# Optimization experiments

Measured on AMD Instinct MI355X. Metric: run time of the kernel, lower is better.

Reference implementation:

```python
import jax, jax.numpy as jnp
import numpy as np

MAX_DISP = 48
PATCH = 3
OFFSET = 0
PAD = PATCH // 2
EPS = 1e-3


def _unfold(x, P, pad):
    # x: [B,C,H,W] -> [B,C,K2,H,W], K2 enumerated row-major over the PxP window
    B, C, H, W = x.shape
    xp = jnp.pad(x, ((0, 0), (0, 0), (pad, pad), (pad, pad)))
    return jnp.stack([xp[:, :, i:i + H, j:j + W]
                      for i in range(P) for j in range(P)], axis=2)


def _normalize(x, axes):
    # torch F.normalize: x / clamp(||x||_2, min=eps)
    n = jnp.sqrt(jnp.sum(x * x, axis=axes, keepdims=True))
    return x / jnp.maximum(n, EPS)


def setup_inputs() -> dict:
    key = jax.random.key(0)
    k1, k2, k3 = jax.random.split(key, 3)
    shp = (2, 32, 128, 416)
    return {
        "xl": jax.random.normal(k1, shp, dtype=jnp.float32),
        "xm": jax.random.normal(k2, shp, dtype=jnp.float32),
        "xr": jax.random.normal(k3, shp, dtype=jnp.float32),
    }


def reference(xl, xm, xr):
    B, C, H, W = xl.shape
    K2 = PATCH * PATCH
    scale = (C * K2) ** 0.5

    pl = _normalize(_unfold(xl, PATCH, PAD), (1, 2))  # [B,C,K2,H,W]
    pr = _normalize(_unfold(xr, PATCH, PAD), (1, 2))
    fl = _normalize(xm, (1,))                          # [B,C,H,W]

    # fl is constant over the K2 axis, so sum patches over K2 once for sim_L/sim_R
    Sl = pl.sum(axis=2)  # [B,C,H,W]
    Sr = pr.sum(axis=2)

    cL, cR, cLR = [], [], []
    for d in range(OFFSET, OFFSET + MAX_DISP):
        if d > 0:
            # shifted_l[w] = patches_l[w+d] (zero right pad); shifted_r[w] = patches_r[w-d]
            sL = jnp.einsum('bchw,bchw->bhw', fl[..., :W - d], Sl[..., d:])
            sL = jnp.pad(sL, ((0, 0), (0, 0), (0, d)))
            sR = jnp.einsum('bchw,bchw->bhw', fl[..., d:], Sr[..., :W - d])
            sR = jnp.pad(sR, ((0, 0), (0, 0), (d, 0)))
            wlr = W - 2 * d  # overlap region of the two opposite shifts
            if wlr > 0:
                sLR = jnp.einsum('bckhw,bckhw->bhw', pl[..., 2 * d:], pr[..., :wlr])
                sLR = jnp.pad(sLR, ((0, 0), (0, 0), (d, d)))
            else:
                sLR = jnp.zeros((B, H, W), xl.dtype)
        else:
            sL = jnp.einsum('bchw,bchw->bhw', fl, Sl)
            sR = jnp.einsum('bchw,bchw->bhw', fl, Sr)
            sLR = jnp.einsum('bckhw,bckhw->bhw', pl, pr)
        cL.append(sL / scale)
        cR.append(sR / scale)
        cLR.append(sLR / scale)

    cost = jnp.stack([jnp.stack(cL, 1), jnp.stack(cR, 1), jnp.stack(cLR, 1)], axis=1)
    return jnp.clip(cost, -10.0, 10.0).astype(jnp.float16)  # [B,3,D,H,W]
```

## Files before the change

### kernel.cpp

```cpp
#include <hip/hip_runtime.h>
#include <math.h>

#define B 2
#define C 32
#define H 128
#define W 416
#define D 48
#define HW (H*W)
#define CHW (C*HW)
#define EPSN 1e-3f
#define ISCALE 0.05892556509887896f
#define ESTR 36
#define DSPL (D / 2)

typedef _Float16 h16;
typedef _Float16 __attribute__((ext_vector_type(2))) h16x2;

__device__ __forceinline__ float clip10(float x) {
    return fminf(fmaxf(x, -10.0f), 10.0f);
}

__device__ __forceinline__ float fdot2(h16x2 a, h16x2 bb, float c) {
    return __builtin_amdgcn_fdot2(a, bb, c, false);
}
__device__ __forceinline__ h16x2 u2h(unsigned int u) {
    union { unsigned int u; h16x2 h; } cv; cv.u = u; return cv.h;
}
__device__ __forceinline__ unsigned int pkh(float a, float bb) {
    union { h16x2 h; unsigned int u; } cv;
    cv.h = h16x2{(h16)a, (h16)bb}; return cv.u;
}

#define FMA4(acc, f, k, u) acc += f[4*(k)+0]*(u).x + f[4*(k)+1]*(u).y \
                               + f[4*(k)+2]*(u).z + f[4*(k)+3]*(u).w;

#define CLW(v) ((v) < 0 ? 0 : ((v) > (W - 1) ? (W - 1) : (v)))

__global__ __launch_bounds__(256) void k_norm(const float* __restrict__ sql,
                                              const float* __restrict__ sqr,
                                              float* __restrict__ inl,
                                              float* __restrict__ inr) {
    int idx = blockIdx.x * 256 + threadIdx.x;
    if (idx >= B * HW) return;
    int b = idx / HW, hw = idx - b * HW;
    int h = hw / W, w = hw - h * W;
    float sl = 0.f, sr = 0.f;
#pragma unroll
    for (int di = -1; di <= 1; ++di) {
        int hh = h + di;
        if (hh < 0 || hh >= H) continue;
#pragma unroll
        for (int dj = -1; dj <= 1; ++dj) {
            int ww = w + dj;
            if (ww < 0 || ww >= W) continue;
            int p = b * HW + hh * W + ww;
            sl += sql[p];
            sr += sqr[p];
        }
    }
    inl[idx] = 1.0f / fmaxf(sqrtf(sl), EPSN);
    inr[idx] = 1.0f / fmaxf(sqrtf(sr), EPSN);
}

__device__ __forceinline__ void stage_row_v2(const float* __restrict__ gsrc,
                                             float* __restrict__ lds,
                                             int tid, int nthreads) {
    for (int t = tid; t < (W / 4) * C; t += nthreads) {
        int rw = t & 7;
        int cl = (t >> 3) & 7;
        int g  = t >> 6;
        int wg = g % 13;
        int ch = g / 13;
        int c  = ch * 8 + cl;
        int w4 = (wg * 8 + rw) * 4;
        float4 v = *(const float4*)(gsrc + (size_t)c * HW + w4);
        lds[(w4 + 0) * ESTR + c] = v.x;
        lds[(w4 + 1) * ESTR + c] = v.y;
        lds[(w4 + 2) * ESTR + c] = v.z;
        lds[(w4 + 3) * ESTR + c] = v.w;
    }
}

__device__ __forceinline__ void stage_row3_h(const float* __restrict__ gsrc,
                                             unsigned int* __restrict__ lds,
                                             int h, int tid, int nthreads) {
    for (int t = tid; t < (W / 4) * (C / 2); t += nthreads) {
        int p = t & 15;
        int u = t >> 4;
        int v0 = 4 * u;
        const float* pa = gsrc + (size_t)(2 * p) * HW + v0;
        const float* pb = pa + HW;
        float4 va = *(const float4*)pa;
        float4 vb = *(const float4*)pb;
        if (h > 0) {
            float4 xa = *(const float4*)(pa - W);
            float4 xb = *(const float4*)(pb - W);
            va.x += xa.x; va.y += xa.y; va.z += xa.z; va.w += xa.w;
            vb.x += xb.x; vb.y += xb.y; vb.z += xb.z; vb.w += xb.w;
        }
        if (h < H - 1) {
            float4 xa = *(const float4*)(pa + W);
            float4 xb = *(const float4*)(pb + W);
            va.x += xa.x; va.y += xa.y; va.z += xa.z; va.w += xa.w;
            vb.x += xb.x; vb.y += xb.y; vb.z += xb.z; vb.w += xb.w;
        }
        int q = p >> 2, lo = p & 3;
        unsigned int pk0 = pkh(va.x, vb.x);
        unsigned int pk1 = pkh(va.y, vb.y);
        unsigned int pk2 = pkh(va.z, vb.z);
        unsigned int pk3 = pkh(va.w, vb.w);
#define PUTH(vv, val) { int _v = (vv); \
    lds[16 * (_v ^ ((_v >> 1) & 1)) \
        + 4 * (q ^ ((((_v) >> 1) ^ ((_v) >> 2)) & 3)) + lo] = (val); }
        PUTH(v0 + 0, pk0)
        PUTH(v0 + 1, pk1)
        PUTH(v0 + 2, pk2)
        PUTH(v0 + 3, pk3)
#undef PUTH
    }
}

__device__ __forceinline__ float dot32e(const float* __restrict__ x,
                                        const float* __restrict__ col) {
    const float4* c4 = (const float4*)col;
    float4 u0 = c4[0], u1 = c4[1], u2 = c4[2], u3 = c4[3];
    float4 u4 = c4[4], u5 = c4[5], u6 = c4[6], u7 = c4[7];
    float a = 0.f, bb = 0.f;
    FMA4(a, x, 0, u0) FMA4(a, x, 1, u1) FMA4(a, x, 2, u2) FMA4(a, x, 3, u3)
    FMA4(bb, x, 4, u4) FMA4(bb, x, 5, u5) FMA4(bb, x, 6, u6) FMA4(bb, x, 7, u7)
    return a + bb;
}

__global__ __launch_bounds__(256) void k_lr(const float* __restrict__ xm,
                                            const float* __restrict__ xl,
                                            const float* __restrict__ xr,
                                            const float* __restrict__ inl,
                                            const float* __restrict__ inr,
                                            float* __restrict__ out) {
    __shared__ unsigned int sBu[W * 16];
    __shared__ float sIn[W];
    int tid = threadIdx.x;
    int h = blockIdx.x;
    int b = blockIdx.y;
    int d0 = blockIdx.z * DSPL;
    bool act = tid < (W / 2);
    int w = 2 * tid;
    int bhw = b * HW + h * W;
    const float* pm = xm + (size_t)b * CHW + h * W;

    h16x2 f0h[16], f1h[16];
    if (act) {
        float t0[C], t1[C];
        float am0 = 0.f, am1 = 0.f;
#pragma unroll
        for (int c = 0; c < C; ++c) {
            float2 mv = *(const float2*)(pm + (size_t)c * HW + w);
            t0[c] = mv.x; t1[c] = mv.y;
            am0 += mv.x * mv.x; am1 += mv.y * mv.y;
        }
        float im0 = 1.0f / fmaxf(sqrtf(am0), EPSN);
        float im1 = 1.0f / fmaxf(sqrtf(am1), EPSN);
#pragma unroll
        for (int j = 0; j < 16; ++j) {
            f0h[j] = h16x2{(h16)(t0[2 * j] * im0), (h16)(t0[2 * j + 1] * im0)};
            f1h[j] = h16x2{(h16)(t1[2 * j] * im1), (h16)(t1[2 * j + 1] * im1)};
        }
    } else {
#pragma unroll
        for (int j = 0; j < 16; ++j) { f0h[j] = h16x2{(h16)0.f, (h16)0.f};
                                       f1h[j] = h16x2{(h16)0.f, (h16)0.f}; }
    }

    uint4 RA0, RA1, RA2, RA3;
    uint4 RB0, RB1, RB2, RB3;

#define LOADH(P, vv) { int _v = CLW(vv); \
    const uint4* _c4 = (const uint4*)(sBu + 16 * (_v ^ ((_v >> 1) & 1))); \
    int _ky = ((_v >> 1) ^ (_v >> 2)) & 3; \
    P##0 = _c4[_ky]; P##1 = _c4[1 ^ _ky]; P##2 = _c4[2 ^ _ky]; P##3 = _c4[3 ^ _ky]; }

#define DOTH(P, c0, c1) { \
    float _a0 = 0.f, _a1 = 0.f, _b0 = 0.f, _b1 = 0.f; \
    _a0 = fdot2(f0h[0],  u2h((P##0).x), _a0); _a0 = fdot2(f0h[1],  u2h((P##0).y), _a0); \
    _a0 = fdot2(f0h[2],  u2h((P##0).z), _a0); _a0 = fdot2(f0h[3],  u2h((P##0).w), _a0); \
    _a0 = fdot2(f0h[4],  u2h((P##1).x), _a0); _a0 = fdot2(f0h[5],  u2h((P##1).y), _a0); \
    _a0 = fdot2(f0h[6],  u2h((P##1).z), _a0); _a0 = fdot2(f0h[7],  u2h((P##1).w), _a0); \
    _a1 = fdot2(f0h[8],  u2h((P##2).x), _a1); _a1 = fdot2(f0h[9],  u2h((P##2).y), _a1); \
    _a1 = fdot2(f0h[10], u2h((P##2).z), _a1); _a1 = fdot2(f0h[11], u2h((P##2).w), _a1); \
    _a1 = fdot2(f0h[12], u2h((P##3).x), _a1); _a1 = fdot2(f0h[13], u2h((P##3).y), _a1); \
    _a1 = fdot2(f0h[14], u2h((P##3).z), _a1); _a1 = fdot2(f0h[15], u2h((P##3).w), _a1); \
    _b0 = fdot2(f1h[0],  u2h((P##0).x), _b0); _b0 = fdot2(f1h[1],  u2h((P##0).y), _b0); \
    _b0 = fdot2(f1h[2],  u2h((P##0).z), _b0); _b0 = fdot2(f1h[3],  u2h((P##0).w), _b0); \
    _b0 = fdot2(f1h[4],  u2h((P##1).x), _b0); _b0 = fdot2(f1h[5],  u2h((P##1).y), _b0); \
    _b0 = fdot2(f1h[6],  u2h((P##1).z), _b0); _b0 = fdot2(f1h[7],  u2h((P##1).w), _b0); \
    _b1 = fdot2(f1h[8],  u2h((P##2).x), _b1); _b1 = fdot2(f1h[9],  u2h((P##2).y), _b1); \
    _b1 = fdot2(f1h[10], u2h((P##2).z), _b1); _b1 = fdot2(f1h[11], u2h((P##2).w), _b1); \
    _b1 = fdot2(f1h[12], u2h((P##3).x), _b1); _b1 = fdot2(f1h[13], u2h((P##3).y), _b1); \
    _b1 = fdot2(f1h[14], u2h((P##3).z), _b1); _b1 = fdot2(f1h[15], u2h((P##3).w), _b1); \
    c0 = _a0 + _a1; c1 = _b0 + _b1; }

    stage_row3_h(xl + (size_t)b * CHW + h * W, sBu, h, tid, 256);
    for (int j = tid; j < W; j += 256) sIn[j] = inl[bhw + j];
    __syncthreads();
    if (act) {
        float* oL = out + ((size_t)b * 3 + 0) * D * HW + h * W;
        const int vb = w + d0 - 1;
        float g0a = 0.f, g0b = 0.f, g1a = 0.f, g1b = 0.f, s0p = 0.f;
#define STEPL(P, jj) { int v = vb + (jj); bool ok = (v >= 0) && (v < W); \
    float c0, c1; DOTH(P, c0, c1); c0 = ok ? c0 : 0.f; c1 = ok ? c1 : 0.f; \
    float s0 = 0.f, s1 = 0.f; \
    if ((jj) >= 2) { int m = v - 1; \
        if (m < W) { float sc = sIn[m] * ISCALE; \
            s0 = clip10((g0a + g0b + c0) * sc); s1 = clip10((g1a + g1b + c1) * sc); } \
        if ((jj) >= 3) { int d = d0 + (jj) - 3; \
            *(float2*)(oL + (size_t)d * HW + w) = make_float2(s0p, s1); } } \
    s0p = s0; g0a = g0b; g0b = c0; g1a = g1b; g1b = c1; }
        LOADH(RA, vb);
#pragma unroll 2
        for (int j = 0; j < DSPL + 2; j += 2) {
            LOADH(RB, vb + j + 1);
            STEPL(RA, j);
            LOADH(RA, vb + j + 2);
            STEPL(RB, j + 1);
        }
        STEPL(RA, DSPL + 2);
#undef STEPL
    }
    __syncthreads();

    stage_row3_h(xr + (size_t)b * CHW + h * W, sBu, h, tid, 256);
    for (int j = tid; j < W; j += 256) sIn[j] = inr[bhw + j];
    __syncthreads();
    if (act) {
        float* oR = out + ((size_t)b * 3 + 1) * D * HW + h * W;
        const int vb = w - d0 - DSPL;
        float g0a = 0.f, g0b = 0.f, g1a = 0.f, g1b = 0.f, s0p = 0.f;
#define STEPR(P, jj) { int v = vb + (jj); bool ok = (v >= 0) && (v < W); \
    float c0, c1; DOTH(P, c0, c1); c0 = ok ? c0 : 0.f; c1 = ok ? c1 : 0.f; \
    float s0 = 0.f, s1 = 0.f; \
    if ((jj) >= 2) { int m = v - 1; \
        if (m >= 0) { float sc = sIn[m] * ISCALE; \
            s0 = clip10((g0a + g0b + c0) * sc); s1 = clip10((g1a + g1b + c1) * sc); } \
        if ((jj) >= 3) { int d = d0 + DSPL + 2 - (jj); \
            *(float2*)(oR + (size_t)d * HW + w) = make_float2(s0p, s1); } } \
    s0p = s0; g0a = g0b; g0b = c0; g1a = g1b; g1b = c1; }
        LOADH(RA, vb);
#pragma unroll 2
        for (int j = 0; j < DSPL + 2; j += 2) {
            LOADH(RB, vb + j + 1);
            STEPR(RA, j);
            LOADH(RA, vb + j + 2);
            STEPR(RB, j + 1);
        }
        STEPR(RA, DSPL + 2);
#undef STEPR
    }
#undef LOADH
#undef DOTH
}

__global__ __launch_bounds__(448, 4) void k_e(const float* __restrict__ xl,
                                              const float* __restrict__ xr,
                                              _Float16* __restrict__ EH,
                                              float* __restrict__ sql,
                                              float* __restrict__ sqr) {
    __shared__ float sXL[W * ESTR];
    int tid = threadIdx.x;
    int h = blockIdx.x;
    int b = blockIdx.y;
    int d0 = blockIdx.z * DSPL;
    int lane = tid & 63;
    int wv = tid >> 6;
    int v = wv * 62 + lane - 1;
    bool vin = (v >= 0) && (v < W);
    const float* br = xr + (size_t)b * CHW + h * W;

    float xrv[C];
#pragma unroll
    for (int c = 0; c < C; ++c) xrv[c] = vin ? br[c * HW + v] : 0.0f;

    stage_row_v2(xl + (size_t)b * CHW + h * W, sXL, tid, 448);
    __syncthreads();

    bool wr = (lane >= 1) && (lane <= 62) && (v < W);

    if (blockIdx.z == 0) {
        float sr_ = 0.f, sl_ = 0.f;
#pragma unroll
        for (int c = 0; c < C; ++c) sr_ += xrv[c] * xrv[c];
        if (vin) {
            const float4* c4 = (const float4*)(sXL + v * ESTR);
#pragma unroll
            for (int q = 0; q < 8; ++q) {
                float4 x = c4[q];
                sl_ += x.x * x.x + x.y * x.y + x.z * x.z + x.w * x.w;
            }
        }
        if (wr) {
            sqr[b * HW + h * W + v] = sr_;
            sql[b * HW + h * W + v] = sl_;
        }
    }

    _Float16* pe = EH + (((size_t)b * D) * H + h) * W + v;

    float4 RA0, RA1, RA2, RA3, RA4, RA5, RA6, RA7;
    float4 RB0, RB1, RB2, RB3, RB4, RB5, RB6, RB7;

#define LOADE(P, col) { int _vq = CLW(col); \
    const float4* _c4 = (const float4*)(sXL + (size_t)_vq * ESTR); \
    P##0 = _c4[0]; P##1 = _c4[1]; P##2 = _c4[2]; P##3 = _c4[3]; \
    P##4 = _c4[4]; P##5 = _c4[5]; P##6 = _c4[6]; P##7 = _c4[7]; }
#define STEPE(P, dd) { float _a = 0.f, _b = 0.f; \
    FMA4(_a, xrv, 0, P##0) FMA4(_a, xrv, 1, P##1) FMA4(_a, xrv, 2, P##2) FMA4(_a, xrv, 3, P##3) \
    FMA4(_b, xrv, 4, P##4) FMA4(_b, xrv, 5, P##5) FMA4(_b, xrv, 6, P##6) FMA4(_b, xrv, 7, P##7) \
    float e = (vin && (v + 2 * (dd)) < W) ? (_a + _b) : 0.f; \
    float em = __shfl_up(e, 1); \
    float ep = __shfl_down(e, 1); \
    float eh = em + e + ep; \
    if (wr) pe[(size_t)(dd) * HW] = (_Float16)eh; }

    LOADE(RA, v + 2 * d0);
#pragma unroll 2
    for (int d = d0; d < d0 + DSPL; d += 2) {
        LOADE(RB, v + 2 * d + 2);
        STEPE(RA, d);
        LOADE(RA, v + 2 * d + 4);
        STEPE(RB, d + 1);
    }
#undef LOADE
#undef STEPE
}

#define DCH 12
__global__ __launch_bounds__(448) void k_lr2(const _Float16* __restrict__ EH,
                                             const float* __restrict__ inl,
                                             const float* __restrict__ inr,
                                             float* __restrict__ out) {
    int w = threadIdx.x;
    int dc = blockIdx.x;
    int h = blockIdx.y;
    int b = blockIdx.z;
    if (w >= W) return;
    int bhw = b * HW + h * W;
    bool hm = (h > 0), hp = (h < H - 1);

    float* o = out + ((size_t)b * 3 + 2) * D * HW + h * W + w;
#pragma unroll
    for (int i = 0; i < DCH; ++i) {
        int d = dc * DCH + i;
        float r = 0.0f;
        if (w >= d && w + d < W) {
            int vc = w - d;
            const _Float16* base = EH + ((size_t)b * D + d) * HW + vc;
            float e = (float)base[h * W];
            if (hm) e += (float)base[(h - 1) * W];
            if (hp) e += (float)base[(h + 1) * W];
            float nl = inl[bhw + w + d];
            float nr = inr[bhw + vc];
            r = clip10(e * nl * nr * ISCALE);
        }
        o[(size_t)d * HW] = r;
    }
}

extern "C" void kernel_launch(void* const* d_in, const int* in_sizes, int n_in,
                              void* d_out, int out_size, void* d_ws, size_t ws_size,
                              hipStream_t stream) {
    const float* xl = (const float*)d_in[0];
    const float* xm = (const float*)d_in[1];
    const float* xr = (const float*)d_in[2];
    float* out = (float*)d_out;

    float* ws = (float*)d_ws;
    float* inl = ws;
    float* inr = inl + B * HW;
    float* sql = inr + B * HW;
    float* sqr = sql + B * HW;
    _Float16* EH = (_Float16*)(sqr + B * HW);

    k_e<<<dim3(H, B, 2), dim3(448), 0, stream>>>(xl, xr, EH, sql, sqr);
    k_norm<<<dim3((B * HW + 255) / 256), dim3(256), 0, stream>>>(sql, sqr, inl, inr);
    k_lr<<<dim3(H, B, 2), dim3(256), 0, stream>>>(xm, xl, xr, inl, inr, out);
    k_lr2<<<dim3(4, H, B), dim3(448), 0, stream>>>(EH, inl, inr, out);
}
```

Baseline: 164.3 us.

## Split k_lr into two 256-thread groups computing left and right costs concurrently

k_lr now launches 512 threads per block. It stages both the left and right row patches and their inverse norms into separate shared buffers behind a single barrier. Thread group 0 computes the left-shift cost and group 1 the right-shift cost in parallel, where before they ran one after the other with a restage in between. This removes two barriers and the serial second pass, but doubles shared memory per block, makes each thread recompute the xm normalization, and may lower occupancy through register pressure at launch bounds 512.

```diff
diff --git a/kernel.cpp b/kernel.cpp
--- a/kernel.cpp
+++ b/kernel.cpp
@@ -131,20 +131,24 @@
     return a + bb;
 }
 
-__global__ __launch_bounds__(256) void k_lr(const float* __restrict__ xm,
+__global__ __launch_bounds__(512) void k_lr(const float* __restrict__ xm,
                                             const float* __restrict__ xl,
                                             const float* __restrict__ xr,
                                             const float* __restrict__ inl,
                                             const float* __restrict__ inr,
                                             float* __restrict__ out) {
-    __shared__ unsigned int sBu[W * 16];
-    __shared__ float sIn[W];
+    __shared__ unsigned int sBuL[W * 16];
+    __shared__ unsigned int sBuR[W * 16];
+    __shared__ float sInL[W];
+    __shared__ float sInR[W];
     int tid = threadIdx.x;
+    int grp = tid >> 8;
+    int t8 = tid & 255;
     int h = blockIdx.x;
     int b = blockIdx.y;
     int d0 = blockIdx.z * DSPL;
-    bool act = tid < (W / 2);
-    int w = 2 * tid;
+    bool act = t8 < (W / 2);
+    int w = 2 * t8;
     int bhw = b * HW + h * W;
     const float* pm = xm + (size_t)b * CHW + h * W;
 
@@ -171,11 +175,19 @@
                                        f1h[j] = h16x2{(h16)0.f, (h16)0.f}; }
     }
 
+    stage_row3_h(xl + (size_t)b * CHW + h * W, sBuL, h, tid, 512);
+    stage_row3_h(xr + (size_t)b * CHW + h * W, sBuR, h, tid, 512);
+    for (int j = tid; j < W; j += 512) {
+        sInL[j] = inl[bhw + j];
+        sInR[j] = inr[bhw + j];
+    }
+    __syncthreads();
+
     uint4 RA0, RA1, RA2, RA3;
     uint4 RB0, RB1, RB2, RB3;
 
-#define LOADH(P, vv) { int _v = CLW(vv); \
-    const uint4* _c4 = (const uint4*)(sBu + 16 * (_v ^ ((_v >> 1) & 1))); \
+#define LOADH(P, buf, vv) { int _v = CLW(vv); \
+    const uint4* _c4 = (const uint4*)((buf) + 16 * (_v ^ ((_v >> 1) & 1))); \
     int _ky = ((_v >> 1) ^ (_v >> 2)) & 3; \
     P##0 = _c4[_ky]; P##1 = _c4[1 ^ _ky]; P##2 = _c4[2 ^ _ky]; P##3 = _c4[3 ^ _ky]; }
 
@@ -199,10 +211,7 @@
     _b1 = fdot2(f1h[14], u2h((P##3).z), _b1); _b1 = fdot2(f1h[15], u2h((P##3).w), _b1); \
     c0 = _a0 + _a1; c1 = _b0 + _b1; }
 
-    stage_row3_h(xl + (size_t)b * CHW + h * W, sBu, h, tid, 256);
-    for (int j = tid; j < W; j += 256) sIn[j] = inl[bhw + j];
-    __syncthreads();
-    if (act) {
+    if (act && grp == 0) {
         float* oL = out + ((size_t)b * 3 + 0) * D * HW + h * W;
         const int vb = w + d0 - 1;
         float g0a = 0.f, g0b = 0.f, g1a = 0.f, g1b = 0.f, s0p = 0.f;
@@ -210,28 +219,22 @@
     float c0, c1; DOTH(P, c0, c1); c0 = ok ? c0 : 0.f; c1 = ok ? c1 : 0.f; \
     float s0 = 0.f, s1 = 0.f; \
     if ((jj) >= 2) { int m = v - 1; \
-        if (m < W) { float sc = sIn[m] * ISCALE; \
+        if (m < W) { float sc = sInL[m] * ISCALE; \
             s0 = clip10((g0a + g0b + c0) * sc); s1 = clip10((g1a + g1b + c1) * sc); } \
         if ((jj) >= 3) { int d = d0 + (jj) - 3; \
             *(float2*)(oL + (size_t)d * HW + w) = make_float2(s0p, s1); } } \
     s0p = s0; g0a = g0b; g0b = c0; g1a = g1b; g1b = c1; }
-        LOADH(RA, vb);
+        LOADH(RA, sBuL, vb);
 #pragma unroll 2
         for (int j = 0; j < DSPL + 2; j += 2) {
-            LOADH(RB, vb + j + 1);
+            LOADH(RB, sBuL, vb + j + 1);
             STEPL(RA, j);
-            LOADH(RA, vb + j + 2);
+            LOADH(RA, sBuL, vb + j + 2);
             STEPL(RB, j + 1);
         }
         STEPL(RA, DSPL + 2);
 #undef STEPL
-    }
-    __syncthreads();
-
-    stage_row3_h(xr + (size_t)b * CHW + h * W, sBu, h, tid, 256);
-    for (int j = tid; j < W; j += 256) sIn[j] = inr[bhw + j];
-    __syncthreads();
-    if (act) {
+    } else if (act) {
         float* oR = out + ((size_t)b * 3 + 1) * D * HW + h * W;
         const int vb = w - d0 - DSPL;
         float g0a = 0.f, g0b = 0.f, g1a = 0.f, g1b = 0.f, s0p = 0.f;
@@ -239,17 +242,17 @@
     float c0, c1; DOTH(P, c0, c1); c0 = ok ? c0 : 0.f; c1 = ok ? c1 : 0.f; \
     float s0 = 0.f, s1 = 0.f; \
     if ((jj) >= 2) { int m = v - 1; \
-        if (m >= 0) { float sc = sIn[m] * ISCALE; \
+        if (m >= 0) { float sc = sInR[m] * ISCALE; \
             s0 = clip10((g0a + g0b + c0) * sc); s1 = clip10((g1a + g1b + c1) * sc); } \
         if ((jj) >= 3) { int d = d0 + DSPL + 2 - (jj); \
             *(float2*)(oR + (size_t)d * HW + w) = make_float2(s0p, s1); } } \
     s0p = s0; g0a = g0b; g0b = c0; g1a = g1b; g1b = c1; }
-        LOADH(RA, vb);
+        LOADH(RA, sBuR, vb);
 #pragma unroll 2
         for (int j = 0; j < DSPL + 2; j += 2) {
-            LOADH(RB, vb + j + 1);
+            LOADH(RB, sBuR, vb + j + 1);
             STEPR(RA, j);
-            LOADH(RA, vb + j + 2);
+            LOADH(RA, sBuR, vb + j + 2);
             STEPR(RB, j + 1);
         }
         STEPR(RA, DSPL + 2);
@@ -381,6 +384,6 @@
 
     k_e<<<dim3(H, B, 2), dim3(448), 0, stream>>>(xl, xr, EH, sql, sqr);
     k_norm<<<dim3((B * HW + 255) / 256), dim3(256), 0, stream>>>(sql, sqr, inl, inr);
-    k_lr<<<dim3(H, B, 2), dim3(256), 0, stream>>>(xm, xl, xr, inl, inr, out);
+    k_lr<<<dim3(H, B, 2), dim3(512), 0, stream>>>(xm, xl, xr, inl, inr, out);
     k_lr2<<<dim3(4, H, B), dim3(448), 0, stream>>>(EH, inl, inr, out);
 }
```

Result: no change. 161.9 us (-1.5%).
